# Kernel optimization log

Hardware: AMD Instinct MI355X
Metric: run time of the kernel (lower is better)

## Reference

```python
import jax, jax.numpy as jnp
import numpy as np

N = 8192
IN_F = 512
OUT_F = 64
NEG_SLOPE = 0.01  # nn.LeakyReLU default
MASK_VAL = -1e9


def setup_inputs() -> dict:
    key = jax.random.key(0)
    k_h, k_adj, k_W, k_a = jax.random.split(key, 4)
    h = jax.random.normal(k_h, (N, IN_F), dtype=jnp.float32)
    adjacency = jax.random.randint(k_adj, (N, N), 0, 2, dtype=jnp.int32)
    # xavier_uniform bounds
    bW = float(np.sqrt(6.0 / (IN_F + OUT_F)))
    ba = float(np.sqrt(6.0 / (2 * OUT_F + 1)))
    W = jax.random.uniform(k_W, (IN_F, OUT_F), minval=-bW, maxval=bW, dtype=jnp.float32)
    a = jax.random.uniform(k_a, (2 * OUT_F, 1), minval=-ba, maxval=ba, dtype=jnp.float32)
    return {"h": h, "adjacency": adjacency, "W": W, "a": a}


def reference(h, adjacency, W, a):
    WH = h @ W                                  # [N, out_f]
    wh1 = WH @ a[:OUT_F, :]                     # [N, 1]
    wh2 = WH @ a[OUT_F:, :]                     # [N, 1]
    e = jax.nn.leaky_relu(wh1 + wh2.T, negative_slope=NEG_SLOPE)  # [N, N]
    attnt = jnp.where(adjacency > 0, e, jnp.float32(MASK_VAL))
    attnt = jax.nn.softmax(attnt, axis=1)       # row-wise softmax
    hfirst = attnt @ WH                         # [N, out_f]
    return jax.nn.elu(hfirst)
```

## Files before the change

kernel.cpp:

```cpp
#include <hip/hip_runtime.h>
#include <hip/hip_bf16.h>

#define N 8192
#define IN_F 512
#define OUT_F 64
#define S_SPLIT 16
#define JT (N / S_SPLIT)
#define NB (N / 8)

typedef __attribute__((ext_vector_type(8))) short short8;
typedef __attribute__((ext_vector_type(4))) float floatx4;
typedef __attribute__((ext_vector_type(4))) int intx4;

__device__ inline short f2bf(float x) {
    __hip_bfloat16 b = __float2bfloat16(x);
    return __builtin_bit_cast(short, b);
}

__global__ __launch_bounds__(256) void k_pack(const int* __restrict__ adj,
                                              unsigned* __restrict__ mask) {
    int t = blockIdx.x * 256 + threadIdx.x;
    const int* p = adj + (size_t)t * 32;
    unsigned b = 0;
#pragma unroll
    for (int c = 0; c < 8; c++) {
        intx4 v = *(const intx4*)(p + c * 4);
#pragma unroll
        for (int j = 0; j < 4; j++)
            b |= (v[j] > 0 ? 1u : 0u) << (c * 4 + j);
    }
    mask[t] = b;
}

__global__ void k_wt(const float* __restrict__ W, short* __restrict__ WT) {
    int idx = blockIdx.x * 256 + threadIdx.x;
    int k = idx >> 6, f = idx & 63;
    WT[f * IN_F + k] = f2bf(W[k * OUT_F + f]);
}

__global__ __launch_bounds__(64) void k_wh(const float* __restrict__ h,
                                           const short* __restrict__ WT,
                                           float* __restrict__ WH,
                                           short* __restrict__ WHbT) {
    __shared__ float tile[OUT_F][17];
    int lane = threadIdx.x;
    int n = lane & 15, q = lane >> 4;
    int i0 = blockIdx.x * 16;
    int rowA = i0 + n;
    const float* hp = h + (size_t)rowA * IN_F + q * 8;
    floatx4 acc[4] = {};
    for (int k0 = 0; k0 < IN_F; k0 += 32) {
        floatx4 h0 = *(const floatx4*)(hp + k0);
        floatx4 h1 = *(const floatx4*)(hp + k0 + 4);
        short8 af;
#pragma unroll
        for (int j = 0; j < 4; j++) { af[j] = f2bf(h0[j]); af[j + 4] = f2bf(h1[j]); }
#pragma unroll
        for (int b = 0; b < 4; b++) {
            short8 bf_ = *(const short8*)(WT + (b * 16 + n) * IN_F + k0 + q * 8);
            acc[b] = __builtin_amdgcn_mfma_f32_16x16x32_bf16(af, bf_, acc[b], 0, 0, 0);
        }
    }
#pragma unroll
    for (int b = 0; b < 4; b++) {
#pragma unroll
        for (int r = 0; r < 4; r++) {
            int rl = q * 4 + r;
            int col = b * 16 + n;
            float v = acc[b][r];
            WH[(i0 + rl) * OUT_F + col] = v;
            tile[col][rl] = v;
        }
    }
    __syncthreads();
    const float* tc = tile[lane];
    short8 s0, s1;
#pragma unroll
    for (int k = 0; k < 8; k++) { s0[k] = f2bf(tc[k]); s1[k] = f2bf(tc[k + 8]); }
    *(short8*)(WHbT + (size_t)lane * N + i0) = s0;
    *(short8*)(WHbT + (size_t)lane * N + i0 + 8) = s1;
}

__global__ void k_wh12(const float* __restrict__ WH, const float* __restrict__ a,
                       float* __restrict__ wh1, float* __restrict__ wh2) {
    int row = blockIdx.x * 256 + threadIdx.x;
    float s1 = 0.f, s2 = 0.f;
#pragma unroll 8
    for (int f = 0; f < OUT_F; f++) {
        float v = WH[row * OUT_F + f];
        s1 += v * a[f];
        s2 += v * a[OUT_F + f];
    }
    wh1[row] = s1;
    wh2[row] = s2;
}

__global__ __launch_bounds__(256, 4) void k_attn(const unsigned char* __restrict__ mask,
                                                 const short* __restrict__ WHbT,
                                                 const float* __restrict__ wh1,
                                                 const float* __restrict__ wh2,
                                                 float* __restrict__ num_part,
                                                 float* __restrict__ den_part) {
    int w = threadIdx.x >> 6;
    int lane = threadIdx.x & 63;
    int n = lane & 15, q = lane >> 4;
    int i0 = blockIdx.x * 64 + w * 16;
    int rowA = i0 + n;
    int split = blockIdx.y;
    int j0 = split * JT;

    const intx4* mp = (const intx4*)(mask + (size_t)rowA * NB + (j0 >> 3));
    intx4 mdw0 = mp[0], mdw1 = mp[1], mdw2 = mp[2], mdw3 = mp[3];

    const float* w2p = wh2 + j0 + q * 8;
    const short* bp0 = WHbT + (size_t)n * N + j0 + q * 8;
    float my_wh1 = wh1[rowA];

    floatx4 acc[4] = {};
    float dsum = 0.f;
    int qs = q * 8;

#pragma unroll
    for (int s = 0; s < 16; s++) {
        unsigned md = (unsigned)((s < 4) ? mdw0[s] : (s < 8) ? mdw1[s - 4]
                               : (s < 12) ? mdw2[s - 8] : mdw3[s - 12]);
        floatx4 w20 = *(const floatx4*)(w2p + s * 32);
        floatx4 w21 = *(const floatx4*)(w2p + s * 32 + 4);
        short8 bfr[4];
#pragma unroll
        for (int b = 0; b < 4; b++)
            bfr[b] = *(const short8*)(bp0 + (size_t)b * 16 * N + s * 32);

        float p[8];
#pragma unroll
        for (int jj = 0; jj < 8; jj++) {
            float e = my_wh1 + ((jj < 4) ? w20[jj] : w21[jj - 4]);
            float el = fmaxf(e, 0.01f * e);
            float pv = __expf(el);
            pv = ((md >> (qs + jj)) & 1u) ? pv : 0.f;
            p[jj] = pv;
            dsum += pv;
        }
        short8 af;
#pragma unroll
        for (int jj = 0; jj < 8; jj++) af[jj] = f2bf(p[jj]);
#pragma unroll
        for (int b = 0; b < 4; b++)
            acc[b] = __builtin_amdgcn_mfma_f32_16x16x32_bf16(af, bfr[b], acc[b], 0, 0, 0);
    }

    dsum += __shfl_xor(dsum, 16, 64);
    dsum += __shfl_xor(dsum, 32, 64);
    if (q == 0) den_part[(size_t)split * N + rowA] = dsum;

    float* np_ = num_part + (size_t)split * N * OUT_F;
#pragma unroll
    for (int b = 0; b < 4; b++)
#pragma unroll
        for (int r = 0; r < 4; r++)
            np_[(i0 + q * 4 + r) * OUT_F + b * 16 + n] = acc[b][r];
}

__global__ void k_final(const float* __restrict__ num_part,
                        const float* __restrict__ den_part,
                        float* __restrict__ out) {
    int idx = blockIdx.x * 256 + threadIdx.x;
    int row = idx >> 6;
    float s = 0.f, d = 0.f;
#pragma unroll
    for (int sp = 0; sp < S_SPLIT; sp++) {
        s += num_part[(size_t)sp * N * OUT_F + idx];
        d += den_part[sp * N + row];
    }
    float x = s / d;
    out[idx] = (x > 0.f) ? x : (__expf(x) - 1.f);
}

extern "C" void kernel_launch(void* const* d_in, const int* in_sizes, int n_in,
                              void* d_out, int out_size, void* d_ws, size_t ws_size,
                              hipStream_t stream) {
    const float* h = (const float*)d_in[0];
    const int* adj = (const int*)d_in[1];
    const float* W = (const float*)d_in[2];
    const float* a = (const float*)d_in[3];
    float* out = (float*)d_out;

    char* ws = (char*)d_ws;
    float* WH       = (float*)(ws);
    short* WHbT     = (short*)(ws + (size_t)(2 << 20));
    short* WT       = (short*)(ws + (size_t)(3 << 20));
    float* wh1      = (float*)(ws + (size_t)(3 << 20) + (64 << 10));
    float* wh2      = wh1 + N;
    unsigned* maskb = (unsigned*)(ws + (size_t)(4 << 20));
    float* num_p    = (float*)(ws + (size_t)(16 << 20));
    float* den_p    = (float*)(ws + (size_t)(48 << 20));

    k_pack<<<dim3((N / 8 * N / 4) / 256), dim3(256), 0, stream>>>(adj, maskb);
    k_wt<<<dim3(128), dim3(256), 0, stream>>>(W, WT);
    k_wh<<<dim3(N / 16), dim3(64), 0, stream>>>(h, WT, WH, WHbT);
    k_wh12<<<dim3(N / 256), dim3(256), 0, stream>>>(WH, a, wh1, wh2);
    k_attn<<<dim3(128, S_SPLIT), dim3(256), 0, stream>>>((const unsigned char*)maskb,
                                                         WHbT, wh1, wh2, num_p, den_p);
    k_final<<<dim3((N * OUT_F) / 256), dim3(256), 0, stream>>>(num_p, den_p, out);
}
```

Before: 460.8 us.

## Stage WH tile in LDS for 64-row attention blocks and fuse wh1/wh2 into k_wh

The attention kernel now copies the per-split WHbT slab (64 features × 512 columns) into padded LDS once per block. Each wave then handles 64 rows (four 16-row fragments) instead of 16, so every B fragment is reused four times and global/L2 traffic for WHbT drops. The wh1/wh2 projections are computed inside k_wh with shuffles, which removes the fp32 WH buffer and the separate k_wh12 launch. In exchange, accumulator registers grow fourfold (64 floats per lane), the grid shrinks to 32x16 blocks, and about 66 KB of LDS per block limits occupancy.

```diff
diff --git a/kernel.cpp b/kernel.cpp
--- a/kernel.cpp
+++ b/kernel.cpp
@@ -7,6 +7,7 @@
 #define S_SPLIT 16
 #define JT (N / S_SPLIT)
 #define NB (N / 8)
+#define LDP 520
 
 typedef __attribute__((ext_vector_type(8))) short short8;
 typedef __attribute__((ext_vector_type(4))) float floatx4;
@@ -40,8 +41,10 @@
 
 __global__ __launch_bounds__(64) void k_wh(const float* __restrict__ h,
                                            const short* __restrict__ WT,
-                                           float* __restrict__ WH,
-                                           short* __restrict__ WHbT) {
+                                           const float* __restrict__ a,
+                                           short* __restrict__ WHbT,
+                                           float* __restrict__ wh1,
+                                           float* __restrict__ wh2) {
     __shared__ float tile[OUT_F][17];
     int lane = threadIdx.x;
     int n = lane & 15, q = lane >> 4;
@@ -62,103 +65,129 @@
         }
     }
 #pragma unroll
-    for (int b = 0; b < 4; b++) {
-#pragma unroll
-        for (int r = 0; r < 4; r++) {
-            int rl = q * 4 + r;
-            int col = b * 16 + n;
-            float v = acc[b][r];
-            WH[(i0 + rl) * OUT_F + col] = v;
-            tile[col][rl] = v;
+    for (int b = 0; b < 4; b++)
+#pragma unroll
+        for (int r = 0; r < 4; r++)
+            tile[b * 16 + n][q * 4 + r] = acc[b][r];
+    float a1v[4], a2v[4];
+#pragma unroll
+    for (int b = 0; b < 4; b++) { a1v[b] = a[b * 16 + n]; a2v[b] = a[OUT_F + b * 16 + n]; }
+#pragma unroll
+    for (int r = 0; r < 4; r++) {
+        float s1 = 0.f, s2 = 0.f;
+#pragma unroll
+        for (int b = 0; b < 4; b++) { s1 += acc[b][r] * a1v[b]; s2 += acc[b][r] * a2v[b]; }
+#pragma unroll
+        for (int m = 1; m <= 8; m <<= 1) {
+            s1 += __shfl_xor(s1, m, 64);
+            s2 += __shfl_xor(s2, m, 64);
+        }
+        if (n == 0) {
+            wh1[i0 + q * 4 + r] = s1;
+            wh2[i0 + q * 4 + r] = s2;
         }
     }
     __syncthreads();
     const float* tc = tile[lane];
-    short8 s0, s1;
-#pragma unroll
-    for (int k = 0; k < 8; k++) { s0[k] = f2bf(tc[k]); s1[k] = f2bf(tc[k + 8]); }
+    short8 s0, s1v;
+#pragma unroll
+    for (int k = 0; k < 8; k++) { s0[k] = f2bf(tc[k]); s1v[k] = f2bf(tc[k + 8]); }
     *(short8*)(WHbT + (size_t)lane * N + i0) = s0;
-    *(short8*)(WHbT + (size_t)lane * N + i0 + 8) = s1;
-}
-
-__global__ void k_wh12(const float* __restrict__ WH, const float* __restrict__ a,
-                       float* __restrict__ wh1, float* __restrict__ wh2) {
-    int row = blockIdx.x * 256 + threadIdx.x;
-    float s1 = 0.f, s2 = 0.f;
-#pragma unroll 8
-    for (int f = 0; f < OUT_F; f++) {
-        float v = WH[row * OUT_F + f];
-        s1 += v * a[f];
-        s2 += v * a[OUT_F + f];
-    }
-    wh1[row] = s1;
-    wh2[row] = s2;
-}
-
-__global__ __launch_bounds__(256, 4) void k_attn(const unsigned char* __restrict__ mask,
-                                                 const short* __restrict__ WHbT,
-                                                 const float* __restrict__ wh1,
-                                                 const float* __restrict__ wh2,
-                                                 float* __restrict__ num_part,
-                                                 float* __restrict__ den_part) {
-    int w = threadIdx.x >> 6;
-    int lane = threadIdx.x & 63;
+    *(short8*)(WHbT + (size_t)lane * N + i0 + 8) = s1v;
+}
+
+__global__ __launch_bounds__(256) void k_attn(const unsigned char* __restrict__ mask,
+                                              const short* __restrict__ WHbT,
+                                              const float* __restrict__ wh1,
+                                              const float* __restrict__ wh2,
+                                              float* __restrict__ num_part,
+                                              float* __restrict__ den_part) {
+    __shared__ short ldsb[OUT_F * LDP];
+    int tid = threadIdx.x;
+    int w = tid >> 6;
+    int lane = tid & 63;
     int n = lane & 15, q = lane >> 4;
-    int i0 = blockIdx.x * 64 + w * 16;
-    int rowA = i0 + n;
     int split = blockIdx.y;
     int j0 = split * JT;
-
-    const intx4* mp = (const intx4*)(mask + (size_t)rowA * NB + (j0 >> 3));
-    intx4 mdw0 = mp[0], mdw1 = mp[1], mdw2 = mp[2], mdw3 = mp[3];
-
+    int i0 = blockIdx.x * 256 + w * 64;
+
+#pragma unroll
+    for (int l = 0; l < 16; l++) {
+        int idx = l * 256 + tid;
+        int f = idx >> 6, c16 = idx & 63;
+        short8 v = *(const short8*)(WHbT + (size_t)f * N + j0 + c16 * 8);
+        *(short8*)(ldsb + f * LDP + c16 * 8) = v;
+    }
+    __syncthreads();
+
+    intx4 mrf[4];
+    float wh1f[4];
+#pragma unroll
+    for (int rf = 0; rf < 4; rf++) {
+        int rowA = i0 + rf * 16 + n;
+        wh1f[rf] = wh1[rowA];
+    }
+
+    floatx4 acc[4][4] = {};
+    float dsum[4] = {0.f, 0.f, 0.f, 0.f};
     const float* w2p = wh2 + j0 + q * 8;
-    const short* bp0 = WHbT + (size_t)n * N + j0 + q * 8;
-    float my_wh1 = wh1[rowA];
-
-    floatx4 acc[4] = {};
-    float dsum = 0.f;
+    const short* lp = ldsb + q * 8;
     int qs = q * 8;
 
-#pragma unroll
-    for (int s = 0; s < 16; s++) {
-        unsigned md = (unsigned)((s < 4) ? mdw0[s] : (s < 8) ? mdw1[s - 4]
-                               : (s < 12) ? mdw2[s - 8] : mdw3[s - 12]);
-        floatx4 w20 = *(const floatx4*)(w2p + s * 32);
-        floatx4 w21 = *(const floatx4*)(w2p + s * 32 + 4);
-        short8 bfr[4];
+    for (int g = 0; g < 4; g++) {
+#pragma unroll
+        for (int rf = 0; rf < 4; rf++) {
+            int rowA = i0 + rf * 16 + n;
+            mrf[rf] = *(const intx4*)(mask + (size_t)rowA * NB + split * 64 + g * 16);
+        }
+#pragma unroll
+        for (int d = 0; d < 4; d++) {
+            int s = g * 4 + d;
+            floatx4 w20 = *(const floatx4*)(w2p + s * 32);
+            floatx4 w21 = *(const floatx4*)(w2p + s * 32 + 4);
+            short8 bfr[4];
+#pragma unroll
+            for (int b = 0; b < 4; b++)
+                bfr[b] = *(const short8*)(lp + (b * 16 + n) * LDP + s * 32);
+#pragma unroll
+            for (int rf = 0; rf < 4; rf++) {
+                unsigned md = (unsigned)mrf[rf][d];
+                float p[8];
+#pragma unroll
+                for (int jj = 0; jj < 8; jj++) {
+                    float e = wh1f[rf] + ((jj < 4) ? w20[jj] : w21[jj - 4]);
+                    float el = fmaxf(e, 0.01f * e);
+                    float pv = __expf(el);
+                    pv = ((md >> (qs + jj)) & 1u) ? pv : 0.f;
+                    p[jj] = pv;
+                    dsum[rf] += pv;
+                }
+                short8 af;
+#pragma unroll
+                for (int jj = 0; jj < 8; jj++) af[jj] = f2bf(p[jj]);
+#pragma unroll
+                for (int b = 0; b < 4; b++)
+                    acc[rf][b] = __builtin_amdgcn_mfma_f32_16x16x32_bf16(af, bfr[b], acc[rf][b], 0, 0, 0);
+            }
+        }
+    }
+
+#pragma unroll
+    for (int rf = 0; rf < 4; rf++) {
+        float d = dsum[rf];
+        d += __shfl_xor(d, 16, 64);
+        d += __shfl_xor(d, 32, 64);
+        if (q == 0) den_part[(size_t)split * N + i0 + rf * 16 + n] = d;
+    }
+
+    float* np_ = num_part + (size_t)split * N * OUT_F;
+#pragma unroll
+    for (int rf = 0; rf < 4; rf++)
 #pragma unroll
         for (int b = 0; b < 4; b++)
-            bfr[b] = *(const short8*)(bp0 + (size_t)b * 16 * N + s * 32);
-
-        float p[8];
-#pragma unroll
-        for (int jj = 0; jj < 8; jj++) {
-            float e = my_wh1 + ((jj < 4) ? w20[jj] : w21[jj - 4]);
-            float el = fmaxf(e, 0.01f * e);
-            float pv = __expf(el);
-            pv = ((md >> (qs + jj)) & 1u) ? pv : 0.f;
-            p[jj] = pv;
-            dsum += pv;
-        }
-        short8 af;
-#pragma unroll
-        for (int jj = 0; jj < 8; jj++) af[jj] = f2bf(p[jj]);
-#pragma unroll
-        for (int b = 0; b < 4; b++)
-            acc[b] = __builtin_amdgcn_mfma_f32_16x16x32_bf16(af, bfr[b], acc[b], 0, 0, 0);
-    }
-
-    dsum += __shfl_xor(dsum, 16, 64);
-    dsum += __shfl_xor(dsum, 32, 64);
-    if (q == 0) den_part[(size_t)split * N + rowA] = dsum;
-
-    float* np_ = num_part + (size_t)split * N * OUT_F;
-#pragma unroll
-    for (int b = 0; b < 4; b++)
-#pragma unroll
-        for (int r = 0; r < 4; r++)
-            np_[(i0 + q * 4 + r) * OUT_F + b * 16 + n] = acc[b][r];
+#pragma unroll
+            for (int r = 0; r < 4; r++)
+                np_[(size_t)(i0 + rf * 16 + q * 4 + r) * OUT_F + b * 16 + n] = acc[rf][b][r];
 }
 
 __global__ void k_final(const float* __restrict__ num_part,
@@ -186,20 +215,18 @@
     float* out = (float*)d_out;
 
     char* ws = (char*)d_ws;
-    float* WH       = (float*)(ws);
-    short* WHbT     = (short*)(ws + (size_t)(2 << 20));
-    short* WT       = (short*)(ws + (size_t)(3 << 20));
-    float* wh1      = (float*)(ws + (size_t)(3 << 20) + (64 << 10));
+    short* WHbT     = (short*)(ws);
+    short* WT       = (short*)(ws + (size_t)(1 << 20));
+    float* wh1      = (float*)(ws + (size_t)(1 << 20) + (64 << 10));
     float* wh2      = wh1 + N;
-    unsigned* maskb = (unsigned*)(ws + (size_t)(4 << 20));
+    unsigned* maskb = (unsigned*)(ws + (size_t)(2 << 20));
     float* num_p    = (float*)(ws + (size_t)(16 << 20));
     float* den_p    = (float*)(ws + (size_t)(48 << 20));
 
-    k_pack<<<dim3((N / 8 * N / 4) / 256), dim3(256), 0, stream>>>(adj, maskb);
+    k_pack<<<dim3((N / 32) * (N / 256)), dim3(256), 0, stream>>>(adj, maskb);
     k_wt<<<dim3(128), dim3(256), 0, stream>>>(W, WT);
-    k_wh<<<dim3(N / 16), dim3(64), 0, stream>>>(h, WT, WH, WHbT);
-    k_wh12<<<dim3(N / 256), dim3(256), 0, stream>>>(WH, a, wh1, wh2);
-    k_attn<<<dim3(128, S_SPLIT), dim3(256), 0, stream>>>((const unsigned char*)maskb,
-                                                         WHbT, wh1, wh2, num_p, den_p);
+    k_wh<<<dim3(N / 16), dim3(64), 0, stream>>>(h, WT, a, WHbT, wh1, wh2);
+    k_attn<<<dim3(N / 256, S_SPLIT), dim3(256), 0, stream>>>((const unsigned char*)maskb,
+                                                             WHbT, wh1, wh2, num_p, den_p);
     k_final<<<dim3((N * OUT_F) / 256), dim3(256), 0, stream>>>(num_p, den_p, out);
 }
```

After: 420.6 us. 1.1x faster.
